# Performance work log

Hardware: AMD Instinct MI355X
Metric: run time of the kernel (lower is better)

## Reference

```python
import jax, jax.numpy as jnp
import numpy as np

IN_DIM, OUT_DIM, RANK = 4096, 4096, 16

def setup_inputs() -> dict:
    key = jax.random.key(0)
    k_x, k_w, k_a, k_b = jax.random.split(key, 4)
    x = jax.random.normal(k_x, (8, 2048, IN_DIM), dtype=jnp.float32)
    weight = jax.random.normal(k_w, (OUT_DIM, IN_DIM), dtype=jnp.float32)
    bias = jnp.zeros((OUT_DIM,), dtype=jnp.float32)
    # orthogonal-ish init for A, B via QR on gaussian
    A = jnp.linalg.qr(jax.random.normal(k_a, (IN_DIM, RANK), dtype=jnp.float32))[0]
    B = jnp.linalg.qr(jax.random.normal(k_b, (OUT_DIM, RANK), dtype=jnp.float32))[0].T
    return {"x": x, "A": A, "B": B, "weight": weight, "bias": bias}

def reference(x, A, B, weight, bias):
    # eval-mode dropout == identity, so
    # x @ (weight.T + A@B) + bias == x@weight.T + (x@A)@B + bias (fused low-rank path)
    base = jnp.einsum('bsd,od->bso', x, weight)
    lora = jnp.einsum('bsr,ro->bso', jnp.einsum('bsd,dr->bsr', x, A), B)
    return base + lora + bias
```

## Files before the change

### kernel.cpp

```cpp
#include <hip/hip_runtime.h>
#include <hip/hip_bf16.h>
#include <cstdint>

#define M_DIM 16384
#define K_DIM 4096
#define N_DIM 4096
#define RANK  16

#define BM 128
#define BN 128
#define BK 32

typedef __bf16 bf16x8 __attribute__((ext_vector_type(8)));
typedef float  f32x4  __attribute__((ext_vector_type(4)));

__device__ __forceinline__ uint16_t f2bf(float f) {
    union { float f; uint32_t u; } v; v.f = f;
    uint32_t u = v.u;
    return (uint16_t)((u + 0x7FFFu + ((u >> 16) & 1u)) >> 16);
}

__global__ void cvt_x_kernel(const float* __restrict__ x, uint16_t* __restrict__ xb) {
    size_t g = (size_t)blockIdx.x * blockDim.x + threadIdx.x;
    const float4* xv = (const float4*)x;
    float4 a = xv[2 * g];
    float4 b = xv[2 * g + 1];
    union { uint4 u; uint16_t h[8]; } p;
    p.h[0] = f2bf(a.x); p.h[1] = f2bf(a.y); p.h[2] = f2bf(a.z); p.h[3] = f2bf(a.w);
    p.h[4] = f2bf(b.x); p.h[5] = f2bf(b.y); p.h[6] = f2bf(b.z); p.h[7] = f2bf(b.w);
    ((uint4*)xb)[g] = p.u;
}

__global__ void prep_w_kernel(const float* __restrict__ W, const float* __restrict__ A,
                              const float* __restrict__ B, uint16_t* __restrict__ wb) {
    const int n = blockIdx.x;
    __shared__ float bcol[RANK];
    if (threadIdx.x < RANK) bcol[threadIdx.x] = B[threadIdx.x * N_DIM + n];
    __syncthreads();
    float bc[RANK];
#pragma unroll
    for (int r = 0; r < RANK; r++) bc[r] = bcol[r];

    for (int k = threadIdx.x; k < K_DIM; k += blockDim.x) {
        const float4* ar = (const float4*)(A + (size_t)k * RANK);
        float acc = W[(size_t)n * K_DIM + k];
#pragma unroll
        for (int q = 0; q < 4; q++) {
            float4 a4 = ar[q];
            acc += a4.x * bc[4*q+0] + a4.y * bc[4*q+1] + a4.z * bc[4*q+2] + a4.w * bc[4*q+3];
        }
        wb[(size_t)n * K_DIM + k] = f2bf(acc);
    }
}

__device__ __forceinline__ void gload_lds16(const void* g, void* l) {
    __builtin_amdgcn_global_load_lds(
        (const __attribute__((address_space(1))) void*)g,
        (__attribute__((address_space(3))) void*)l,
        16, 0, 0);
}

__global__ __launch_bounds__(256, 2)
void gemm_bt_bias(const uint16_t* __restrict__ Xb,
                  const uint16_t* __restrict__ Wb,
                  const float* __restrict__ bias,
                  float* __restrict__ C) {
    __shared__ uint16_t As[BM * BK];
    __shared__ uint16_t Bs[BN * BK];

    const int tid  = threadIdx.x;
    const int wave = tid >> 6;
    const int lane = tid & 63;

    const int bm = blockIdx.y * BM;
    const int bn = blockIdx.x * BN;

    const int wm = (wave >> 1) * 64;
    const int wn = (wave & 1) * 64;

    const int c0 = tid;
    const int c1 = tid + 256;
    const int r0 = c0 >> 2, q0 = c0 & 3;
    const int r1 = c1 >> 2, q1 = c1 & 3;

    const uint16_t* xg0 = Xb + (size_t)(bm + r0) * K_DIM + q0 * 8;
    const uint16_t* xg1 = Xb + (size_t)(bm + r1) * K_DIM + q1 * 8;
    const uint16_t* wg0 = Wb + (size_t)(bn + r0) * K_DIM + q0 * 8;
    const uint16_t* wg1 = Wb + (size_t)(bn + r1) * K_DIM + q1 * 8;

    uint16_t* lA0 = As + c0 * 8;
    uint16_t* lA1 = As + c1 * 8;
    uint16_t* lB0 = Bs + c0 * 8;
    uint16_t* lB1 = Bs + c1 * 8;

    const int m15 = lane & 15;
    const int kq  = lane >> 4;
    const int koff = kq * 8;

    f32x4 acc[4][4];
    const f32x4 zero = {0.f, 0.f, 0.f, 0.f};
#pragma unroll
    for (int i = 0; i < 4; i++)
#pragma unroll
        for (int j = 0; j < 4; j++) acc[i][j] = zero;

    for (int k0 = 0; k0 < K_DIM; k0 += BK) {
        gload_lds16(xg0 + k0, lA0);
        gload_lds16(xg1 + k0, lA1);
        gload_lds16(wg0 + k0, lB0);
        gload_lds16(wg1 + k0, lB1);
        __syncthreads();

        bf16x8 af[4], bfr[4];
#pragma unroll
        for (int i = 0; i < 4; i++)
            af[i] = *(const bf16x8*)&As[(wm + i * 16 + m15) * BK + koff];
#pragma unroll
        for (int j = 0; j < 4; j++)
            bfr[j] = *(const bf16x8*)&Bs[(wn + j * 16 + m15) * BK + koff];

#pragma unroll
        for (int i = 0; i < 4; i++)
#pragma unroll
            for (int j = 0; j < 4; j++)
                acc[i][j] = __builtin_amdgcn_mfma_f32_16x16x32_bf16(af[i], bfr[j], acc[i][j], 0, 0, 0);

        __syncthreads();
    }

#pragma unroll
    for (int j = 0; j < 4; j++) {
        const int col = bn + wn + j * 16 + m15;
        const float bv = bias[col];
#pragma unroll
        for (int i = 0; i < 4; i++) {
            const int row0 = bm + wm + i * 16 + kq * 4;
#pragma unroll
            for (int r = 0; r < 4; r++) {
                C[(size_t)(row0 + r) * N_DIM + col] = acc[i][j][r] + bv;
            }
        }
    }
}

extern "C" void kernel_launch(void* const* d_in, const int* in_sizes, int n_in,
                              void* d_out, int out_size, void* d_ws, size_t ws_size,
                              hipStream_t stream) {
    const float* x    = (const float*)d_in[0];
    const float* A    = (const float*)d_in[1];
    const float* B    = (const float*)d_in[2];
    const float* W    = (const float*)d_in[3];
    const float* bias = (const float*)d_in[4];
    float* out = (float*)d_out;

    uint16_t* Xb = (uint16_t*)d_ws;
    uint16_t* Wb = (uint16_t*)((char*)d_ws + (size_t)M_DIM * K_DIM * sizeof(uint16_t));

    cvt_x_kernel<<<(M_DIM * K_DIM) / (8 * 256), 256, 0, stream>>>(x, Xb);
    prep_w_kernel<<<N_DIM, 256, 0, stream>>>(W, A, B, Wb);

    dim3 grid(N_DIM / BN, M_DIM / BM);
    gemm_bt_bias<<<grid, 256, 0, stream>>>(Xb, Wb, bias, out);
}
```

Baseline: 1.130 ms.

## Double BK to 64 with XOR-swizzled LDS layout and merge prep kernels

Raises the GEMM K-tile from 32 to 64, halving the number of loop iterations and barrier pairs. The LDS layout gets an XOR swizzle on 16-byte chunks to avoid bank conflicts on the wider rows. The launch-bounds occupancy hint goes from 2 to 3 blocks per CU. The x-conversion and weight-merge kernels become one launch to save a kernel launch. LDS use doubles to 32KB per block, and register pressure may rise under the stricter occupancy target.

```diff
diff --git a/kernel.cpp b/kernel.cpp
--- a/kernel.cpp
+++ b/kernel.cpp
@@ -9,7 +9,7 @@
 
 #define BM 128
 #define BN 128
-#define BK 32
+#define BK 64
 
 typedef __bf16 bf16x8 __attribute__((ext_vector_type(8)));
 typedef float  f32x4  __attribute__((ext_vector_type(4)));
@@ -20,36 +20,38 @@
     return (uint16_t)((u + 0x7FFFu + ((u >> 16) & 1u)) >> 16);
 }
 
-__global__ void cvt_x_kernel(const float* __restrict__ x, uint16_t* __restrict__ xb) {
-    size_t g = (size_t)blockIdx.x * blockDim.x + threadIdx.x;
-    const float4* xv = (const float4*)x;
-    float4 a = xv[2 * g];
-    float4 b = xv[2 * g + 1];
-    union { uint4 u; uint16_t h[8]; } p;
-    p.h[0] = f2bf(a.x); p.h[1] = f2bf(a.y); p.h[2] = f2bf(a.z); p.h[3] = f2bf(a.w);
-    p.h[4] = f2bf(b.x); p.h[5] = f2bf(b.y); p.h[6] = f2bf(b.z); p.h[7] = f2bf(b.w);
-    ((uint4*)xb)[g] = p.u;
-}
+#define CVT_BLOCKS (M_DIM * K_DIM / (8 * 256))
 
-__global__ void prep_w_kernel(const float* __restrict__ W, const float* __restrict__ A,
-                              const float* __restrict__ B, uint16_t* __restrict__ wb) {
-    const int n = blockIdx.x;
-    __shared__ float bcol[RANK];
-    if (threadIdx.x < RANK) bcol[threadIdx.x] = B[threadIdx.x * N_DIM + n];
-    __syncthreads();
-    float bc[RANK];
+__global__ void prep_kernel(const float* __restrict__ x, uint16_t* __restrict__ xb,
+                            const float* __restrict__ W, const float* __restrict__ A,
+                            const float* __restrict__ B, uint16_t* __restrict__ wb) {
+    if (blockIdx.x < CVT_BLOCKS) {
+        size_t g = (size_t)blockIdx.x * blockDim.x + threadIdx.x;
+        const float4* xv = (const float4*)x;
+        float4 a = xv[2 * g];
+        float4 b = xv[2 * g + 1];
+        union { uint4 u; uint16_t h[8]; } p;
+        p.h[0] = f2bf(a.x); p.h[1] = f2bf(a.y); p.h[2] = f2bf(a.z); p.h[3] = f2bf(a.w);
+        p.h[4] = f2bf(b.x); p.h[5] = f2bf(b.y); p.h[6] = f2bf(b.z); p.h[7] = f2bf(b.w);
+        ((uint4*)xb)[g] = p.u;
+    } else {
+        const int n = blockIdx.x - CVT_BLOCKS;
+        __shared__ float bcol[RANK];
+        if (threadIdx.x < RANK) bcol[threadIdx.x] = B[threadIdx.x * N_DIM + n];
+        __syncthreads();
+        float bc[RANK];
 #pragma unroll
-    for (int r = 0; r < RANK; r++) bc[r] = bcol[r];
-
-    for (int k = threadIdx.x; k < K_DIM; k += blockDim.x) {
-        const float4* ar = (const float4*)(A + (size_t)k * RANK);
-        float acc = W[(size_t)n * K_DIM + k];
+        for (int r = 0; r < RANK; r++) bc[r] = bcol[r];
+        for (int k = threadIdx.x; k < K_DIM; k += blockDim.x) {
+            const float4* ar = (const float4*)(A + (size_t)k * RANK);
+            float acc = W[(size_t)n * K_DIM + k];
 #pragma unroll
-        for (int q = 0; q < 4; q++) {
-            float4 a4 = ar[q];
-            acc += a4.x * bc[4*q+0] + a4.y * bc[4*q+1] + a4.z * bc[4*q+2] + a4.w * bc[4*q+3];
+            for (int q = 0; q < 4; q++) {
+                float4 a4 = ar[q];
+                acc += a4.x * bc[4*q+0] + a4.y * bc[4*q+1] + a4.z * bc[4*q+2] + a4.w * bc[4*q+3];
+            }
+            wb[(size_t)n * K_DIM + k] = f2bf(acc);
         }
-        wb[(size_t)n * K_DIM + k] = f2bf(acc);
     }
 }
 
@@ -60,7 +62,7 @@
         16, 0, 0);
 }
 
-__global__ __launch_bounds__(256, 2)
+__global__ __launch_bounds__(256, 3)
 void gemm_bt_bias(const uint16_t* __restrict__ Xb,
                   const uint16_t* __restrict__ Wb,
                   const float* __restrict__ bias,
@@ -78,24 +80,37 @@
     const int wm = (wave >> 1) * 64;
     const int wn = (wave & 1) * 64;
 
-    const int c0 = tid;
-    const int c1 = tid + 256;
-    const int r0 = c0 >> 2, q0 = c0 & 3;
-    const int r1 = c1 >> 2, q1 = c1 & 3;
-
-    const uint16_t* xg0 = Xb + (size_t)(bm + r0) * K_DIM + q0 * 8;
-    const uint16_t* xg1 = Xb + (size_t)(bm + r1) * K_DIM + q1 * 8;
-    const uint16_t* wg0 = Wb + (size_t)(bn + r0) * K_DIM + q0 * 8;
-    const uint16_t* wg1 = Wb + (size_t)(bn + r1) * K_DIM + q1 * 8;
-
-    uint16_t* lA0 = As + c0 * 8;
-    uint16_t* lA1 = As + c1 * 8;
-    uint16_t* lB0 = Bs + c0 * 8;
-    uint16_t* lB1 = Bs + c1 * 8;
+    const uint16_t* xg[4];
+    const uint16_t* wg[4];
+    uint16_t* lA[4];
+    uint16_t* lB[4];
+#pragma unroll
+    for (int s = 0; s < 4; s++) {
+        const int c   = tid + 256 * s;
+        const int row = c >> 3;
+        const int ql  = c & 7;
+        const int qg  = ql ^ (row & 7);
+        xg[s] = Xb + (size_t)(bm + row) * K_DIM + qg * 8;
+        wg[s] = Wb + (size_t)(bn + row) * K_DIM + qg * 8;
+        lA[s] = As + c * 8;
+        lB[s] = Bs + c * 8;
+    }
 
     const int m15 = lane & 15;
     const int kq  = lane >> 4;
-    const int koff = kq * 8;
+
+    int aoff[4][2], boff[4][2];
+#pragma unroll
+    for (int i = 0; i < 4; i++) {
+        const int ra = wm + i * 16 + m15;
+        const int rb = wn + i * 16 + m15;
+#pragma unroll
+        for (int h = 0; h < 2; h++) {
+            const int kc = h * 4 + kq;
+            aoff[i][h] = (ra * 8 + (kc ^ (ra & 7))) * 8;
+            boff[i][h] = (rb * 8 + (kc ^ (rb & 7))) * 8;
+        }
+    }
 
     f32x4 acc[4][4];
     const f32x4 zero = {0.f, 0.f, 0.f, 0.f};
@@ -105,25 +120,25 @@
         for (int j = 0; j < 4; j++) acc[i][j] = zero;
 
     for (int k0 = 0; k0 < K_DIM; k0 += BK) {
-        gload_lds16(xg0 + k0, lA0);
-        gload_lds16(xg1 + k0, lA1);
-        gload_lds16(wg0 + k0, lB0);
-        gload_lds16(wg1 + k0, lB1);
+#pragma unroll
+        for (int s = 0; s < 4; s++) gload_lds16(xg[s] + k0, lA[s]);
+#pragma unroll
+        for (int s = 0; s < 4; s++) gload_lds16(wg[s] + k0, lB[s]);
         __syncthreads();
 
-        bf16x8 af[4], bfr[4];
 #pragma unroll
-        for (int i = 0; i < 4; i++)
-            af[i] = *(const bf16x8*)&As[(wm + i * 16 + m15) * BK + koff];
+        for (int h = 0; h < 2; h++) {
+            bf16x8 af[4], bfr[4];
 #pragma unroll
-        for (int j = 0; j < 4; j++)
-            bfr[j] = *(const bf16x8*)&Bs[(wn + j * 16 + m15) * BK + koff];
-
+            for (int i = 0; i < 4; i++) af[i]  = *(const bf16x8*)&As[aoff[i][h]];
 #pragma unroll
-        for (int i = 0; i < 4; i++)
+            for (int j = 0; j < 4; j++) bfr[j] = *(const bf16x8*)&Bs[boff[j][h]];
 #pragma unroll
-            for (int j = 0; j < 4; j++)
-                acc[i][j] = __builtin_amdgcn_mfma_f32_16x16x32_bf16(af[i], bfr[j], acc[i][j], 0, 0, 0);
+            for (int i = 0; i < 4; i++)
+#pragma unroll
+                for (int j = 0; j < 4; j++)
+                    acc[i][j] = __builtin_amdgcn_mfma_f32_16x16x32_bf16(af[i], bfr[j], acc[i][j], 0, 0, 0);
+        }
 
         __syncthreads();
     }
@@ -156,8 +171,7 @@
     uint16_t* Xb = (uint16_t*)d_ws;
     uint16_t* Wb = (uint16_t*)((char*)d_ws + (size_t)M_DIM * K_DIM * sizeof(uint16_t));
 
-    cvt_x_kernel<<<(M_DIM * K_DIM) / (8 * 256), 256, 0, stream>>>(x, Xb);
-    prep_w_kernel<<<N_DIM, 256, 0, stream>>>(W, A, B, Wb);
+    prep_kernel<<<CVT_BLOCKS + N_DIM, 256, 0, stream>>>(x, Xb, W, A, B, Wb);
 
     dim3 grid(N_DIM / BN, M_DIM / BM);
     gemm_bt_bias<<<grid, 256, 0, stream>>>(Xb, Wb, bias, out);
```

New measurement: 1.030 ms. 1.1x faster.
